# Kernel tuning notes

Measured on AMD Instinct MI355X. Metric: run time of the kernel, lower is better.

## Reference

```python
import jax, jax.numpy as jnp
import numpy as np

EPS = 0.05
N = 33554432  # 2**25 annotation steps


def setup_inputs() -> dict:
    key = jax.random.key(0)
    # categories in 1..5 (cat==0 is a no-op skip in the original loop; excluding it
    # keeps the output length static at N+1)
    annotation_series = jax.random.randint(key, (N,), 1, 6, dtype=jnp.int64 if jax.config.jax_enable_x64 else jnp.int32)
    # learned scalar weights of the six Linear(1,1,bias=False) layers, at their init constants
    return {
        "annotation_series": annotation_series,
        "origin_w": jnp.asarray(0.0, jnp.float32),
        "big_decrease_w": jnp.asarray(-0.3, jnp.float32),
        "decrease_w": jnp.asarray(-0.1, jnp.float32),
        "same_w": jnp.asarray(0.0, jnp.float32),
        "increase_w": jnp.asarray(0.1, jnp.float32),
        "big_increase_w": jnp.asarray(0.3, jnp.float32),
    }


def _change_table(origin_w, bd, d, s, inc, bi):
    sg = jax.lax.stop_gradient  # clamp bounds came from .item() in torch -> detached
    c1 = jnp.minimum(bd, sg(jnp.minimum(0.0, d))) - EPS                 # big decrease
    c2 = jnp.clip(d, sg(bd) + EPS, 0.0 - EPS)                           # decrease
    c3 = s                                                              # same
    c4 = jnp.clip(inc, 0.0 + EPS, sg(bi) - EPS)                         # increase
    c5 = jnp.maximum(bi, sg(jnp.maximum(0.0, inc)) + EPS)               # big increase
    zero = jnp.zeros_like(c1)  # cat 0 unused (inputs restricted to 1..5)
    return jnp.stack([zero, c1, c2, c3, c4, c5])  # [6]


def reference(annotation_series, origin_w, big_decrease_w, decrease_w, same_w, increase_w, big_increase_w):
    table = _change_table(origin_w, big_decrease_w, decrease_w, same_w, increase_w, big_increase_w)
    changes = table[annotation_series]                    # [N] gather from 6-entry LUT
    series = origin_w + jnp.cumsum(changes)               # [N] inclusive prefix sum
    return jnp.concatenate([origin_w[None], series])      # [N+1]
```

## Files before the change

### kernel.cpp

```cpp
#include <hip/hip_runtime.h>

#define EPS_C 0.05f
#define BLOCK 256
#define ITEMS 4
#define CHUNK (BLOCK * ITEMS)
#define SB 1024
#define SB_ITEMS 32

__device__ __forceinline__ void build_table(const float* bd_p, const float* d_p,
                                            const float* s_p, const float* inc_p,
                                            const float* bi_p, float* cs) {
  if (threadIdx.x == 0) {
    float bd = *bd_p, d = *d_p, s = *s_p, inc = *inc_p, bi = *bi_p;
    cs[0] = 0.0f;
    cs[1] = fminf(bd, fminf(0.0f, d)) - EPS_C;
    cs[2] = fminf(fmaxf(d, bd + EPS_C), -EPS_C);
    cs[3] = s;
    cs[4] = fminf(fmaxf(inc, EPS_C), bi - EPS_C);
    cs[5] = fmaxf(bi, fmaxf(0.0f, inc) + EPS_C);
    cs[6] = 0.0f; cs[7] = 0.0f;
  }
}

__global__ __launch_bounds__(BLOCK) void k_reduce(
    const int* __restrict__ ann, const float* bd, const float* d,
    const float* s, const float* inc, const float* bi,
    float* __restrict__ blockSums) {
  __shared__ float cs[8];
  __shared__ float wsum[BLOCK / 64];
  build_table(bd, d, s, inc, bi, cs);
  __syncthreads();

  const int b = blockIdx.x;
  const int t = threadIdx.x;
  const int4* in4 = (const int4*)(ann + (size_t)b * CHUNK);

  int4 v = in4[t];
  float sum = cs[v.x] + cs[v.y] + cs[v.z] + cs[v.w];
#pragma unroll
  for (int off = 32; off >= 1; off >>= 1) sum += __shfl_down(sum, off, 64);

  const int lane = t & 63, wid = t >> 6;
  if (lane == 0) wsum[wid] = sum;
  __syncthreads();
  if (t == 0) {
    float tot = 0.0f;
#pragma unroll
    for (int i = 0; i < BLOCK / 64; ++i) tot += wsum[i];
    blockSums[b] = tot;
  }
}

__global__ __launch_bounds__(SB) void k_scan_sums(
    const float* __restrict__ sums, float* __restrict__ offs, int nb) {
  __shared__ float wsum[SB / 64];
  const int t = threadIdx.x;
  const int lane = t & 63, wid = t >> 6;

  float pre[SB_ITEMS];
  float run = 0.0f;
#pragma unroll
  for (int i = 0; i < SB_ITEMS; ++i) {
    int idx = t * SB_ITEMS + i;
    float v = (idx < nb) ? sums[idx] : 0.0f;
    pre[i] = run;
    run += v;
  }
  float x = run;
#pragma unroll
  for (int off = 1; off < 64; off <<= 1) {
    float y = __shfl_up(x, off, 64);
    if (lane >= off) x += y;
  }
  if (lane == 63) wsum[wid] = x;
  __syncthreads();
  float wexcl = 0.0f;
  for (int i = 0; i < wid; ++i) wexcl += wsum[i];
  float texcl = wexcl + (x - run);
#pragma unroll
  for (int i = 0; i < SB_ITEMS; ++i) {
    int idx = t * SB_ITEMS + i;
    if (idx < nb) offs[idx] = texcl + pre[i];
  }
}

__global__ __launch_bounds__(BLOCK) void k_scan(
    const int* __restrict__ ann, const float* origin, const float* bd,
    const float* d, const float* s, const float* inc, const float* bi,
    const float* __restrict__ offs, float* __restrict__ out, int nb) {
  __shared__ float cs[8];
  __shared__ float wsum[BLOCK / 64];
  build_table(bd, d, s, inc, bi, cs);
  __syncthreads();

  const int b = blockIdx.x;
  const int t = threadIdx.x;
  const size_t base = (size_t)b * CHUNK;
  const int4* in4 = (const int4*)(ann + base);

  int4 v = in4[t];
  float v0 = cs[v.x], v1 = cs[v.y], v2 = cs[v.z], v3 = cs[v.w];
  float run = v0 + v1 + v2 + v3;

  float x = run;
  const int lane = t & 63, wid = t >> 6;
#pragma unroll
  for (int off = 1; off < 64; off <<= 1) {
    float y = __shfl_up(x, off, 64);
    if (lane >= off) x += y;
  }
  if (lane == 63) wsum[wid] = x;
  __syncthreads();
  float wexcl = 0.0f;
  for (int i = 0; i < wid; ++i) wexcl += wsum[i];

  const float off0 = *origin + offs[b] + wexcl + (x - run);

  float4 o;
  o.x = off0;
  o.y = off0 + v0;
  o.z = off0 + v0 + v1;
  o.w = off0 + v0 + v1 + v2;
  ((float4*)(out + base))[t] = o;

  if (b == nb - 1 && t == BLOCK - 1)
    out[(size_t)nb * CHUNK] = off0 + run;
}

extern "C" void kernel_launch(void* const* d_in, const int* in_sizes, int n_in,
                              void* d_out, int out_size, void* d_ws, size_t ws_size,
                              hipStream_t stream) {
  const int*   ann    = (const int*)d_in[0];
  const float* origin = (const float*)d_in[1];
  const float* bd     = (const float*)d_in[2];
  const float* dw     = (const float*)d_in[3];
  const float* sw     = (const float*)d_in[4];
  const float* inc    = (const float*)d_in[5];
  const float* bi     = (const float*)d_in[6];
  float* out = (float*)d_out;

  const int N  = in_sizes[0];
  const int nb = N / CHUNK;

  float* blockSums = (float*)d_ws;
  float* blockOffs = blockSums + nb;

  k_reduce<<<nb, BLOCK, 0, stream>>>(ann, bd, dw, sw, inc, bi, blockSums);
  k_scan_sums<<<1, SB, 0, stream>>>(blockSums, blockOffs, nb);
  k_scan<<<nb, BLOCK, 0, stream>>>(ann, origin, bd, dw, sw, inc, bi,
                                   blockOffs, out, nb);
}
```

Before: 285.7 us.

## Fuse reduce and scan into one cooperative kernel with packed input reuse

Replaces the reduce / scan-sums / scan three-kernel pipeline with a single cooperative kernel. Each block reads its slice of annotations once, keeps them packed as 4-bit nibbles in shared memory, publishes its block sum, grid-syncs, then computes its prefix from earlier block sums and writes the scanned output from the packed data. This is meant to remove the second full read of the input and two kernel launches. In exchange it relies on a grid-wide barrier, hard-codes a per-block slice size that assumes N divides into 8 tiles of 4096 per block, and uses a less coalesced per-thread load pattern.

```diff
diff --git a/kernel.cpp b/kernel.cpp
--- a/kernel.cpp
+++ b/kernel.cpp
@@ -1,130 +1,130 @@
 #include <hip/hip_runtime.h>
+#include <hip/hip_cooperative_groups.h>
+
+namespace cg = cooperative_groups;
 
 #define EPS_C 0.05f
 #define BLOCK 256
-#define ITEMS 4
-#define CHUNK (BLOCK * ITEMS)
-#define SB 1024
-#define SB_ITEMS 32
+#define GRID_G 1024
+#define TILE 4096
+#define ITERS 8
 
-__device__ __forceinline__ void build_table(const float* bd_p, const float* d_p,
-                                            const float* s_p, const float* inc_p,
-                                            const float* bi_p, float* cs) {
+__global__ __launch_bounds__(BLOCK) void k_coop_scan(
+    const int* __restrict__ ann, const float* __restrict__ origin,
+    const float* __restrict__ bd, const float* __restrict__ d,
+    const float* __restrict__ s, const float* __restrict__ inc,
+    const float* __restrict__ bi, float* __restrict__ ws_sums,
+    float* __restrict__ out, int N) {
+  __shared__ float cs[8];
+  __shared__ float wsum[BLOCK / 64];
+  __shared__ float s_base;
+  __shared__ unsigned int pack[ITERS * BLOCK * 2];
+
   if (threadIdx.x == 0) {
-    float bd = *bd_p, d = *d_p, s = *s_p, inc = *inc_p, bi = *bi_p;
+    float bdv = *bd, dv = *d, sv = *s, incv = *inc, biv = *bi;
     cs[0] = 0.0f;
-    cs[1] = fminf(bd, fminf(0.0f, d)) - EPS_C;
-    cs[2] = fminf(fmaxf(d, bd + EPS_C), -EPS_C);
-    cs[3] = s;
-    cs[4] = fminf(fmaxf(inc, EPS_C), bi - EPS_C);
-    cs[5] = fmaxf(bi, fmaxf(0.0f, inc) + EPS_C);
+    cs[1] = fminf(bdv, fminf(0.0f, dv)) - EPS_C;
+    cs[2] = fminf(fmaxf(dv, bdv + EPS_C), -EPS_C);
+    cs[3] = sv;
+    cs[4] = fminf(fmaxf(incv, EPS_C), biv - EPS_C);
+    cs[5] = fmaxf(biv, fmaxf(0.0f, incv) + EPS_C);
     cs[6] = 0.0f; cs[7] = 0.0f;
   }
-}
-
-__global__ __launch_bounds__(BLOCK) void k_reduce(
-    const int* __restrict__ ann, const float* bd, const float* d,
-    const float* s, const float* inc, const float* bi,
-    float* __restrict__ blockSums) {
-  __shared__ float cs[8];
-  __shared__ float wsum[BLOCK / 64];
-  build_table(bd, d, s, inc, bi, cs);
   __syncthreads();
 
-  const int b = blockIdx.x;
-  const int t = threadIdx.x;
-  const int4* in4 = (const int4*)(ann + (size_t)b * CHUNK);
+  const int b = blockIdx.x, t = threadIdx.x;
+  const int lane = t & 63, wid = t >> 6;
+  const int S = N / GRID_G;
+  const size_t base0 = (size_t)b * S;
 
-  int4 v = in4[t];
-  float sum = cs[v.x] + cs[v.y] + cs[v.z] + cs[v.w];
+  float bsum = 0.0f;
+  for (int it = 0; it < ITERS; ++it) {
+    const int4* in4 = (const int4*)(ann + base0 + (size_t)it * TILE);
+    unsigned int w[2] = {0u, 0u};
+    float ssum = 0.0f;
 #pragma unroll
-  for (int off = 32; off >= 1; off >>= 1) sum += __shfl_down(sum, off, 64);
-
-  const int lane = t & 63, wid = t >> 6;
-  if (lane == 0) wsum[wid] = sum;
+    for (int i = 0; i < 4; ++i) {
+      int4 v = in4[t * 4 + i];
+      ssum += cs[v.x] + cs[v.y] + cs[v.z] + cs[v.w];
+      unsigned int nib = (unsigned)v.x | ((unsigned)v.y << 4) |
+                         ((unsigned)v.z << 8) | ((unsigned)v.w << 12);
+      w[i >> 1] |= nib << ((i & 1) * 16);
+    }
+    pack[(it * BLOCK + t) * 2 + 0] = w[0];
+    pack[(it * BLOCK + t) * 2 + 1] = w[1];
+    bsum += ssum;
+  }
+#pragma unroll
+  for (int off = 32; off >= 1; off >>= 1) bsum += __shfl_down(bsum, off, 64);
+  if (lane == 0) wsum[wid] = bsum;
   __syncthreads();
   if (t == 0) {
-    float tot = 0.0f;
+    float tot = wsum[0] + wsum[1] + wsum[2] + wsum[3];
+    __hip_atomic_store(&ws_sums[b], tot, __ATOMIC_RELEASE,
+                       __HIP_MEMORY_SCOPE_AGENT);
+  }
+
+  cg::this_grid().sync();
+
+  float p = 0.0f;
+  for (int i = t; i < b; i += BLOCK)
+    p += __hip_atomic_load(&ws_sums[i], __ATOMIC_ACQUIRE,
+                           __HIP_MEMORY_SCOPE_AGENT);
 #pragma unroll
-    for (int i = 0; i < BLOCK / 64; ++i) tot += wsum[i];
-    blockSums[b] = tot;
-  }
-}
-
-__global__ __launch_bounds__(SB) void k_scan_sums(
-    const float* __restrict__ sums, float* __restrict__ offs, int nb) {
-  __shared__ float wsum[SB / 64];
-  const int t = threadIdx.x;
-  const int lane = t & 63, wid = t >> 6;
-
-  float pre[SB_ITEMS];
-  float run = 0.0f;
-#pragma unroll
-  for (int i = 0; i < SB_ITEMS; ++i) {
-    int idx = t * SB_ITEMS + i;
-    float v = (idx < nb) ? sums[idx] : 0.0f;
-    pre[i] = run;
-    run += v;
-  }
-  float x = run;
-#pragma unroll
-  for (int off = 1; off < 64; off <<= 1) {
-    float y = __shfl_up(x, off, 64);
-    if (lane >= off) x += y;
-  }
-  if (lane == 63) wsum[wid] = x;
+  for (int off = 32; off >= 1; off >>= 1) p += __shfl_down(p, off, 64);
+  if (lane == 0) wsum[wid] = p;
   __syncthreads();
-  float wexcl = 0.0f;
-  for (int i = 0; i < wid; ++i) wexcl += wsum[i];
-  float texcl = wexcl + (x - run);
-#pragma unroll
-  for (int i = 0; i < SB_ITEMS; ++i) {
-    int idx = t * SB_ITEMS + i;
-    if (idx < nb) offs[idx] = texcl + pre[i];
-  }
-}
-
-__global__ __launch_bounds__(BLOCK) void k_scan(
-    const int* __restrict__ ann, const float* origin, const float* bd,
-    const float* d, const float* s, const float* inc, const float* bi,
-    const float* __restrict__ offs, float* __restrict__ out, int nb) {
-  __shared__ float cs[8];
-  __shared__ float wsum[BLOCK / 64];
-  build_table(bd, d, s, inc, bi, cs);
+  if (t == 0) s_base = *origin + wsum[0] + wsum[1] + wsum[2] + wsum[3];
   __syncthreads();
 
-  const int b = blockIdx.x;
-  const int t = threadIdx.x;
-  const size_t base = (size_t)b * CHUNK;
-  const int4* in4 = (const int4*)(ann + base);
+  float carry = s_base;
+  for (int it = 0; it < ITERS; ++it) {
+    unsigned int w0 = pack[(it * BLOCK + t) * 2 + 0];
+    unsigned int w1 = pack[(it * BLOCK + t) * 2 + 1];
+    float vals[16];
+#pragma unroll
+    for (int j = 0; j < 8; ++j) vals[j] = cs[(w0 >> (4 * j)) & 0xF];
+#pragma unroll
+    for (int j = 0; j < 8; ++j) vals[8 + j] = cs[(w1 >> (4 * j)) & 0xF];
 
-  int4 v = in4[t];
-  float v0 = cs[v.x], v1 = cs[v.y], v2 = cs[v.z], v3 = cs[v.w];
-  float run = v0 + v1 + v2 + v3;
+    float run = 0.0f;
+#pragma unroll
+    for (int i = 0; i < 16; ++i) run += vals[i];
 
-  float x = run;
-  const int lane = t & 63, wid = t >> 6;
+    float x = run;
 #pragma unroll
-  for (int off = 1; off < 64; off <<= 1) {
-    float y = __shfl_up(x, off, 64);
-    if (lane >= off) x += y;
+    for (int off = 1; off < 64; off <<= 1) {
+      float y = __shfl_up(x, off, 64);
+      if (lane >= off) x += y;
+    }
+    __syncthreads();
+    if (lane == 63) wsum[wid] = x;
+    __syncthreads();
+    float wexcl = 0.0f, tot = 0.0f;
+#pragma unroll
+    for (int i = 0; i < BLOCK / 64; ++i) {
+      float wv = wsum[i];
+      if (i < wid) wexcl += wv;
+      tot += wv;
+    }
+    const float off0 = carry + wexcl + (x - run);
+
+    float4* out4 = (float4*)(out + base0 + (size_t)it * TILE);
+    float r = off0;
+#pragma unroll
+    for (int i = 0; i < 4; ++i) {
+      float4 o;
+      o.x = r; r += vals[i * 4 + 0];
+      o.y = r; r += vals[i * 4 + 1];
+      o.z = r; r += vals[i * 4 + 2];
+      o.w = r; r += vals[i * 4 + 3];
+      out4[t * 4 + i] = o;
+    }
+    carry += tot;
   }
-  if (lane == 63) wsum[wid] = x;
-  __syncthreads();
-  float wexcl = 0.0f;
-  for (int i = 0; i < wid; ++i) wexcl += wsum[i];
 
-  const float off0 = *origin + offs[b] + wexcl + (x - run);
-
-  float4 o;
-  o.x = off0;
-  o.y = off0 + v0;
-  o.z = off0 + v0 + v1;
-  o.w = off0 + v0 + v1 + v2;
-  ((float4*)(out + base))[t] = o;
-
-  if (b == nb - 1 && t == BLOCK - 1)
-    out[(size_t)nb * CHUNK] = off0 + run;
+  if (b == GRID_G - 1 && t == BLOCK - 1)
+    out[N] = carry;
 }
 
 extern "C" void kernel_launch(void* const* d_in, const int* in_sizes, int n_in,
@@ -138,15 +138,12 @@
   const float* inc    = (const float*)d_in[5];
   const float* bi     = (const float*)d_in[6];
   float* out = (float*)d_out;
+  float* ws_sums = (float*)d_ws;
+  int N = in_sizes[0];
 
-  const int N  = in_sizes[0];
-  const int nb = N / CHUNK;
-
-  float* blockSums = (float*)d_ws;
-  float* blockOffs = blockSums + nb;
-
-  k_reduce<<<nb, BLOCK, 0, stream>>>(ann, bd, dw, sw, inc, bi, blockSums);
-  k_scan_sums<<<1, SB, 0, stream>>>(blockSums, blockOffs, nb);
-  k_scan<<<nb, BLOCK, 0, stream>>>(ann, origin, bd, dw, sw, inc, bi,
-                                   blockOffs, out, nb);
+  void* args[] = {(void*)&ann, (void*)&origin, (void*)&bd, (void*)&dw,
+                  (void*)&sw,  (void*)&inc,    (void*)&bi, (void*)&ws_sums,
+                  (void*)&out, (void*)&N};
+  hipLaunchCooperativeKernel((const void*)k_coop_scan, dim3(GRID_G),
+                             dim3(BLOCK), args, 0, stream);
 }
```

Result: slower. 495.6 us (+73.5%).

## Pack categories to nibbles in reduce pass and fuse block-offset scan into output kernel

Applied to the files above, without the earlier changes.

The reduce pass now also writes each category as a 4-bit nibble to a compact workspace buffer. The output pass reads that buffer instead of re-reading the 32-bit annotation array, which cuts the second read of the input by a factor of eight. The separate single-block scan over block sums is removed; each output block instead sums all preceding block sums itself. Chunks grow to 4096 elements per block, so there are 8192 sums and that redundant prefix work per block stays bounded. The cost is an extra write and read of the packed buffer and quadratic total work summing block sums.

```diff
diff --git a/kernel.cpp b/kernel.cpp
--- a/kernel.cpp
+++ b/kernel.cpp
@@ -2,10 +2,7 @@
 
 #define EPS_C 0.05f
 #define BLOCK 256
-#define ITEMS 4
-#define CHUNK (BLOCK * ITEMS)
-#define SB 1024
-#define SB_ITEMS 32
+#define CHUNK 4096
 
 __device__ __forceinline__ void build_table(const float* bd_p, const float* d_p,
                                             const float* s_p, const float* inc_p,
@@ -22,109 +19,103 @@
   }
 }
 
-__global__ __launch_bounds__(BLOCK) void k_reduce(
+__global__ __launch_bounds__(BLOCK) void k_reduce_pack(
     const int* __restrict__ ann, const float* bd, const float* d,
     const float* s, const float* inc, const float* bi,
-    float* __restrict__ blockSums) {
+    uint2* __restrict__ packed, float* __restrict__ sums) {
   __shared__ float cs[8];
   __shared__ float wsum[BLOCK / 64];
   build_table(bd, d, s, inc, bi, cs);
   __syncthreads();
 
-  const int b = blockIdx.x;
-  const int t = threadIdx.x;
+  const int b = blockIdx.x, t = threadIdx.x;
   const int4* in4 = (const int4*)(ann + (size_t)b * CHUNK);
 
-  int4 v = in4[t];
-  float sum = cs[v.x] + cs[v.y] + cs[v.z] + cs[v.w];
+  unsigned int w0 = 0u, w1 = 0u;
+  float sum = 0.0f;
+#pragma unroll
+  for (int i = 0; i < 4; ++i) {
+    int4 v = in4[t * 4 + i];
+    sum += cs[v.x] + cs[v.y] + cs[v.z] + cs[v.w];
+    unsigned int nib = (unsigned)v.x | ((unsigned)v.y << 4) |
+                       ((unsigned)v.z << 8) | ((unsigned)v.w << 12);
+    if (i < 2) w0 |= nib << ((i & 1) * 16);
+    else       w1 |= nib << ((i & 1) * 16);
+  }
+  packed[(size_t)b * BLOCK + t] = make_uint2(w0, w1);
+
 #pragma unroll
   for (int off = 32; off >= 1; off >>= 1) sum += __shfl_down(sum, off, 64);
-
   const int lane = t & 63, wid = t >> 6;
   if (lane == 0) wsum[wid] = sum;
   __syncthreads();
-  if (t == 0) {
-    float tot = 0.0f;
-#pragma unroll
-    for (int i = 0; i < BLOCK / 64; ++i) tot += wsum[i];
-    blockSums[b] = tot;
-  }
+  if (t == 0) sums[b] = wsum[0] + wsum[1] + wsum[2] + wsum[3];
 }
 
-__global__ __launch_bounds__(SB) void k_scan_sums(
-    const float* __restrict__ sums, float* __restrict__ offs, int nb) {
-  __shared__ float wsum[SB / 64];
-  const int t = threadIdx.x;
+__global__ __launch_bounds__(BLOCK) void k_scan_out(
+    const uint2* __restrict__ packed, const float* __restrict__ sums,
+    const float* __restrict__ origin, const float* bd, const float* d,
+    const float* s, const float* inc, const float* bi,
+    float* __restrict__ out, int nb) {
+  __shared__ float cs[8];
+  __shared__ float wsum[BLOCK / 64];
+  __shared__ float s_base;
+  build_table(bd, d, s, inc, bi, cs);
+  __syncthreads();
+
+  const int b = blockIdx.x, t = threadIdx.x;
   const int lane = t & 63, wid = t >> 6;
 
-  float pre[SB_ITEMS];
+  float p = 0.0f;
+  for (int i = t; i < b; i += BLOCK) p += sums[i];
+#pragma unroll
+  for (int off = 32; off >= 1; off >>= 1) p += __shfl_down(p, off, 64);
+  if (lane == 0) wsum[wid] = p;
+  __syncthreads();
+  if (t == 0) s_base = *origin + wsum[0] + wsum[1] + wsum[2] + wsum[3];
+  __syncthreads();
+
+  uint2 w = packed[(size_t)b * BLOCK + t];
+  float vals[16];
+#pragma unroll
+  for (int j = 0; j < 8; ++j) vals[j] = cs[(w.x >> (4 * j)) & 0xF];
+#pragma unroll
+  for (int j = 0; j < 8; ++j) vals[8 + j] = cs[(w.y >> (4 * j)) & 0xF];
+
   float run = 0.0f;
 #pragma unroll
-  for (int i = 0; i < SB_ITEMS; ++i) {
-    int idx = t * SB_ITEMS + i;
-    float v = (idx < nb) ? sums[idx] : 0.0f;
-    pre[i] = run;
-    run += v;
-  }
+  for (int i = 0; i < 16; ++i) run += vals[i];
+
   float x = run;
 #pragma unroll
   for (int off = 1; off < 64; off <<= 1) {
     float y = __shfl_up(x, off, 64);
     if (lane >= off) x += y;
   }
+  __syncthreads();
   if (lane == 63) wsum[wid] = x;
   __syncthreads();
   float wexcl = 0.0f;
-  for (int i = 0; i < wid; ++i) wexcl += wsum[i];
-  float texcl = wexcl + (x - run);
 #pragma unroll
-  for (int i = 0; i < SB_ITEMS; ++i) {
-    int idx = t * SB_ITEMS + i;
-    if (idx < nb) offs[idx] = texcl + pre[i];
+  for (int i = 0; i < BLOCK / 64; ++i)
+    if (i < wid) wexcl += wsum[i];
+
+  const float off0 = s_base + wexcl + (x - run);
+
+  const size_t base = (size_t)b * CHUNK;
+  float4* out4 = (float4*)(out + base);
+  float r = off0;
+#pragma unroll
+  for (int i = 0; i < 4; ++i) {
+    float4 o;
+    o.x = r; r += vals[i * 4 + 0];
+    o.y = r; r += vals[i * 4 + 1];
+    o.z = r; r += vals[i * 4 + 2];
+    o.w = r; r += vals[i * 4 + 3];
+    out4[t * 4 + i] = o;
   }
-}
-
-__global__ __launch_bounds__(BLOCK) void k_scan(
-    const int* __restrict__ ann, const float* origin, const float* bd,
-    const float* d, const float* s, const float* inc, const float* bi,
-    const float* __restrict__ offs, float* __restrict__ out, int nb) {
-  __shared__ float cs[8];
-  __shared__ float wsum[BLOCK / 64];
-  build_table(bd, d, s, inc, bi, cs);
-  __syncthreads();
-
-  const int b = blockIdx.x;
-  const int t = threadIdx.x;
-  const size_t base = (size_t)b * CHUNK;
-  const int4* in4 = (const int4*)(ann + base);
-
-  int4 v = in4[t];
-  float v0 = cs[v.x], v1 = cs[v.y], v2 = cs[v.z], v3 = cs[v.w];
-  float run = v0 + v1 + v2 + v3;
-
-  float x = run;
-  const int lane = t & 63, wid = t >> 6;
-#pragma unroll
-  for (int off = 1; off < 64; off <<= 1) {
-    float y = __shfl_up(x, off, 64);
-    if (lane >= off) x += y;
-  }
-  if (lane == 63) wsum[wid] = x;
-  __syncthreads();
-  float wexcl = 0.0f;
-  for (int i = 0; i < wid; ++i) wexcl += wsum[i];
-
-  const float off0 = *origin + offs[b] + wexcl + (x - run);
-
-  float4 o;
-  o.x = off0;
-  o.y = off0 + v0;
-  o.z = off0 + v0 + v1;
-  o.w = off0 + v0 + v1 + v2;
-  ((float4*)(out + base))[t] = o;
-
   if (b == nb - 1 && t == BLOCK - 1)
-    out[(size_t)nb * CHUNK] = off0 + run;
+    out[(size_t)nb * CHUNK] = r;
 }
 
 extern "C" void kernel_launch(void* const* d_in, const int* in_sizes, int n_in,
@@ -142,11 +133,10 @@
   const int N  = in_sizes[0];
   const int nb = N / CHUNK;
 
-  float* blockSums = (float*)d_ws;
-  float* blockOffs = blockSums + nb;
+  float* sums   = (float*)d_ws;
+  uint2* packed = (uint2*)((char*)d_ws + 32768);
 
-  k_reduce<<<nb, BLOCK, 0, stream>>>(ann, bd, dw, sw, inc, bi, blockSums);
-  k_scan_sums<<<1, SB, 0, stream>>>(blockSums, blockOffs, nb);
-  k_scan<<<nb, BLOCK, 0, stream>>>(ann, origin, bd, dw, sw, inc, bi,
-                                   blockOffs, out, nb);
+  k_reduce_pack<<<nb, BLOCK, 0, stream>>>(ann, bd, dw, sw, inc, bi, packed, sums);
+  k_scan_out<<<nb, BLOCK, 0, stream>>>(packed, sums, origin, bd, dw, sw, inc, bi,
+                                       out, nb);
 }
```

Result: faster. 274.1 us (-4.1%).
